# Optimization experiments

Hardware: AMD Instinct MI355X
Metric: run time of the kernel (lower is better)

The kernel has to match this reference:

```python
import jax, jax.numpy as jnp
import numpy as np

DX, DZ, DT = 10.0, 10.0, 1.0e-3
NX, NZ = 512, 512
NSTEPS, NREC = 512, 128
DT2 = DT * DT
INV_DXDZ = 1.0 / (DX * DZ)


def setup_inputs() -> dict:
    key = jax.random.key(0)
    k1, k2, k3, k4 = jax.random.split(key, 4)
    # velocity in [1500, 2500] m/s -> CFL stable with dt=1e-3, dx=dz=10
    velocity_model = 1500.0 + 1000.0 * jax.random.uniform(k1, (NX, NZ), dtype=jnp.float32)
    source = jax.random.normal(k2, (NSTEPS,), dtype=jnp.float32)
    rec_x = jax.random.randint(k3, (NREC,), 0, NX)
    rec_z = jax.random.randint(k4, (NREC,), 0, NZ)
    return {
        "velocity_model": velocity_model,
        "source": source,
        "src_x": 256,
        "src_z": 8,
        "rec_x": rec_x,
        "rec_z": rec_z,
    }


def _laplacian(p):
    # 3x3 cross stencil with zero padding, scaled by 1/(dx*dz) -- identical to
    # F.conv2d(p, [[0,1,0],[1,-4,1],[0,1,0]]/(dx*dz), padding=1)
    pp = jnp.pad(p, 1)
    return (pp[:-2, 1:-1] + pp[2:, 1:-1] + pp[1:-1, :-2] + pp[1:-1, 2:] - 4.0 * p) * INV_DXDZ


def reference(velocity_model, source, src_x, src_z, rec_x, rec_z):
    v2_dt2 = velocity_model * velocity_model * DT2  # [nx, nz]

    def step(carry, s_t):
        p, p_old = carry
        p_new = 2.0 * p - p_old + v2_dt2 * _laplacian(p)
        p_new = p_new.at[src_x, src_z].add(s_t * DT2)
        return (p_new, p), p_new[rec_x, rec_z]  # gather all receivers at once

    p0 = jnp.zeros((NX, NZ), dtype=velocity_model.dtype)
    _, recs = jax.lax.scan(step, (p0, p0), source)  # recs: [n_steps, n_rec]
    return recs.T  # seismogram: [n_rec, n_steps]
```

## Files before the change

kernel.cpp:

```cpp
#include <hip/hip_runtime.h>


#define NXd 512
#define NZd 512
#define NSTEPSd 512
#define NRECd 128
#define DT2f 1.0e-6f
#define INVf 1.0e-2f
#define TBk 16
#define TIk 32
#define EXTk 64
#define NTILEk 16
#define PADk 16
#define PWk 544
#define LROWS 66
#define NROUNDS (NSTEPSd / TBk)
#define MAXR 8

__device__ __forceinline__ float dpp_shr1(float x) {
    int v = __builtin_amdgcn_update_dpp(0, __builtin_bit_cast(int, x),
                                        0x138, 0xF, 0xF, false);
    return __builtin_bit_cast(float, v);
}
__device__ __forceinline__ float dpp_shl1(float x) {
    int v = __builtin_amdgcn_update_dpp(0, __builtin_bit_cast(int, x),
                                        0x130, 0xF, 0xF, false);
    return __builtin_bit_cast(float, v);
}

__device__ __forceinline__ float2 ldg_f2(const float2* p) {
    unsigned long long v = __hip_atomic_load(
        (const unsigned long long*)p, __ATOMIC_RELAXED, __HIP_MEMORY_SCOPE_AGENT);
    return __builtin_bit_cast(float2, v);
}
__device__ __forceinline__ float ldg_f1(const float* p) {
    unsigned v = __hip_atomic_load(
        (const unsigned*)p, __ATOMIC_RELAXED, __HIP_MEMORY_SCOPE_AGENT);
    return __builtin_bit_cast(float, v);
}
__device__ __forceinline__ void stg_f2(float2* p, float2 x) {
    __hip_atomic_store((unsigned long long*)p,
                       __builtin_bit_cast(unsigned long long, x),
                       __ATOMIC_RELAXED, __HIP_MEMORY_SCOPE_AGENT);
}

__global__ __launch_bounds__(1024) void fdtd_persist(
    const float* __restrict__ vel, const float* __restrict__ source,
    const int* __restrict__ src_x, const int* __restrict__ src_z,
    const int* __restrict__ rec_x, const int* __restrict__ rec_z,
    float2* __restrict__ PA, float2* __restrict__ PB,
    float* __restrict__ out, unsigned* __restrict__ done)
{
    __shared__ float sb[2][LROWS * EXTk];
    __shared__ int wflag[16 * 16];

    const int tid = threadIdx.x;
    const int w   = tid >> 6;
    const int ez  = tid & 63;
    const int bx = blockIdx.x, by = blockIdx.y;
    const int gx0 = by * TIk;
    const int gz0 = bx * TIk;
    const int ox = gx0 - TBk, oz = gz0 - TBk;
    const int myid = (by * NTILEk + bx) * 32;

    for (int i = tid; i < 34 * 34; i += 1024) {
        const int p = (by * 34 + i / 34) * PWk + (bx * 34 + i % 34);
        stg_f2(&PA[p], make_float2(0.f, 0.f));
        stg_f2(&PB[p], make_float2(0.f, 0.f));
    }

    int nR = 0; int rSlot[MAXR]; int rReg[MAXR];
    for (int r = 0; r < NRECd; ++r) {
        const int er = rec_x[r] - ox, ec = rec_z[r] - oz;
        if (er >= TBk && er < TBk + TIk && ec >= TBk && ec < TBk + TIk &&
            ec == ez && (er >> 2) == w && nR < MAXR) {
            rSlot[nR] = r; rReg[nR] = er & 3; ++nR;
        }
    }
    for (int j = 0; j < nR; ++j) {
        float4* o4 = (float4*)&out[rSlot[j] * NSTEPSd];
        for (int q = 0; q < NSTEPSd / 4; ++q) o4[q] = make_float4(0.f, 0.f, 0.f, 0.f);
    }

    float rV2i[4];
    {
        const int fz = oz + ez;
        #pragma unroll
        for (int i = 0; i < 4; ++i) {
            const int fx = ox + 4 * w + i;
            float v2 = 0.f;
            if (fx >= 0 && fx < NXd && fz >= 0 && fz < NZd) {
                float v = vel[fx * NZd + fz];
                v2 = v * v * (DT2f * INVf);
            }
            rV2i[i] = v2;
        }
    }

    if (w == 0) {
        sb[0][ez] = 0.f;
        sb[0][(LROWS - 1) * EXTk + ez] = 0.f;
        sb[1][ez] = 0.f;
        sb[1][(LROWS - 1) * EXTk + ez] = 0.f;
    }
    if (ez == 0) wflag[w * 16] = 0;

    const int sx = *src_x, sz = *src_z;
    const int exs = sx - ox, ezs = sz - oz;
    const bool srcHere = (exs >= 0 && exs < EXTk && ezs >= 0 && ezs < EXTk) &&
                         (tid == (((exs >> 2) << 6) | ezs));

    const int dxm = max(0, max(ox - sx, sx - (ox + EXTk - 1)));
    const int dzm = max(0, max(oz - sz, sz - (oz + EXTk - 1)));
    const int dman = dxm + dzm;
    const int kAct = dman <= (TBk + 1) ? 0 : (dman - (TBk + 1) + TBk - 1) / TBk;

    const int lane = tid & 63;
    int nb = myid;
    if (lane < 8) {
        const int d = (lane < 4) ? lane : lane + 1;
        const int ny = min(NTILEk - 1, max(0, by + d / 3 - 1));
        const int nx = min(NTILEk - 1, max(0, bx + d % 3 - 1));
        nb = (ny * NTILEk + nx) * 32;
    }

    const int pbase = (gx0 + 4 * w) * PWk + gz0 + ez;
    const int fbase = 4 * w * EXTk + ez;

    __syncthreads();
    if (tid == 0)
        __hip_atomic_store(&done[myid], (unsigned)(kAct + 1),
                           __ATOMIC_RELAXED, __HIP_MEMORY_SCOPE_AGENT);

    int base = 0;

    for (int k = kAct; k < NROUNDS; ++k) {
        const int t0 = TBk * k;

        if (lane < 8) {
            const unsigned tgt = (unsigned)(k + 1);
            for (;;) {
                unsigned seen = __hip_atomic_load(&done[nb], __ATOMIC_RELAXED,
                                                  __HIP_MEMORY_SCOPE_AGENT);
                if (seen >= tgt) break;
                if (seen + 1 < tgt) __builtin_amdgcn_s_sleep(16);
                else                __builtin_amdgcn_s_sleep(1);
            }
        }

        float2* __restrict__ Pin  = (k & 1) ? PB : PA;
        float2* __restrict__ Pout = (k & 1) ? PA : PB;

        float2 co[4];
        #pragma unroll
        for (int i = 0; i < 4; ++i) co[i] = ldg_f2(&Pin[pbase + i * PWk]);
        const float huG = ldg_f1((const float*)&Pin[pbase - PWk]);
        const float hdG = ldg_f1((const float*)&Pin[pbase + 4 * PWk]);

        float rCur[4], rOld[4];
        #pragma unroll
        for (int i = 0; i < 4; ++i) { rCur[i] = co[i].x; rOld[i] = co[i].y; }

        float sv[TBk];
        if (srcHere) {
            #pragma unroll
            for (int s = 0; s < TBk; ++s) sv[s] = source[t0 + s] * DT2f;
        }

        #pragma unroll
        for (int s = 0; s < TBk; ++s) {
            if (s > 0) {
                const int tgt = base + s;
                if (w > 0)
                    while (__hip_atomic_load(&wflag[(w - 1) * 16],
                                             __ATOMIC_ACQUIRE,
                                             __HIP_MEMORY_SCOPE_WORKGROUP) < tgt)
                        __builtin_amdgcn_s_sleep(1);
                if (w < 15)
                    while (__hip_atomic_load(&wflag[(w + 1) * 16],
                                             __ATOMIC_ACQUIRE,
                                             __HIP_MEMORY_SCOPE_WORKGROUP) < tgt)
                        __builtin_amdgcn_s_sleep(1);
            }
            const float* cur = sb[s & 1];
            float* nxt = sb[(s & 1) ^ 1];
            const float up0 = (s == 0) ? huG : cur[fbase];
            const float dn3 = (s == 0) ? hdG : cur[fbase + 5 * EXTk];
            float nv[4];
            #pragma unroll
            for (int i = 0; i < 4; ++i) {
                const float up = (i == 0) ? up0 : rCur[i - 1];
                const float dn = (i == 3) ? dn3 : rCur[i + 1];
                const float lf = dpp_shr1(rCur[i]);
                const float rt = dpp_shl1(rCur[i]);
                const float sum = (up + dn) + (lf + rt);
                const float t4 = __builtin_fmaf(-4.0f, rCur[i], sum);
                const float pm = __builtin_fmaf(2.0f, rCur[i], -rOld[i]);
                nv[i] = __builtin_fmaf(rV2i[i], t4, pm);
            }
            #pragma unroll
            for (int i = 0; i < 4; ++i) {
                rOld[i] = rCur[i];
                rCur[i] = nv[i];
                nxt[fbase + (1 + i) * EXTk] = nv[i];
            }
            if (srcHere) {
                #pragma unroll
                for (int i = 0; i < 4; ++i) {
                    if (i == (exs & 3)) {
                        rCur[i] += sv[s];
                        nxt[(exs + 1) * EXTk + ezs] = rCur[i];
                    }
                }
            }
            if (ez == 0)
                __hip_atomic_store(&wflag[w * 16], base + s + 1,
                                   __ATOMIC_RELEASE, __HIP_MEMORY_SCOPE_WORKGROUP);
            #pragma unroll
            for (int j = 0; j < MAXR; ++j) {
                if (j < nR) {
                    const int rr = rReg[j];
                    const float v = rr == 0 ? rCur[0] : rr == 1 ? rCur[1]
                                  : rr == 2 ? rCur[2] : rCur[3];
                    out[rSlot[j] * NSTEPSd + t0 + s] = v;
                }
            }
        }
        base += TBk;

        if (w >= 4 && w < 12 && ez >= TBk && ez < EXTk - TBk) {
            #pragma unroll
            for (int i = 0; i < 4; ++i)
                stg_f2(&Pout[pbase + i * PWk], make_float2(rCur[i], rOld[i]));
        }

        __syncthreads();
        if (tid == 0)
            __hip_atomic_store(&done[myid], (unsigned)(k + 2),
                               __ATOMIC_RELAXED, __HIP_MEMORY_SCOPE_AGENT);
    }
}

extern "C" void kernel_launch(void* const* d_in, const int* in_sizes, int n_in,
                              void* d_out, int out_size, void* d_ws, size_t ws_size,
                              hipStream_t stream) {
    const float* vel    = (const float*)d_in[0];
    const float* source = (const float*)d_in[1];
    const int*   src_x  = (const int*)d_in[2];
    const int*   src_z  = (const int*)d_in[3];
    const int*   rec_x  = (const int*)d_in[4];
    const int*   rec_z  = (const int*)d_in[5];
    float* out = (float*)d_out;

    const size_t FP = (size_t)PWk * PWk;
    float2* base = (float2*)d_ws;
    float2* PA = base + PWk;
    float2* PB = PA + FP;
    unsigned* DONE = (unsigned*)(PB + FP + PWk);

    hipMemsetAsync(DONE, 0, (size_t)NTILEk * NTILEk * 32 * sizeof(unsigned), stream);

    void* args[] = {(void*)&vel, (void*)&source, (void*)&src_x, (void*)&src_z,
                    (void*)&rec_x, (void*)&rec_z, (void*)&PA, (void*)&PB,
                    (void*)&out, (void*)&DONE};
    hipLaunchCooperativeKernel((void*)fdtd_persist, dim3(NTILEk, NTILEk),
                               dim3(1024), args, 0, stream);
}
```

Before: 392.1 us.

## Replace per-wave LDS flag spinning with block barrier and halo-only LDS exchange

Each wave now writes only its top and bottom rows (the halo rows neighbours need) into a compact LDS slot array, instead of all four rows. The point-to-point wave flags with acquire spin loops are replaced by a __syncthreads after every substep. The receiver-store loop is skipped when a thread owns no receivers. This cuts LDS traffic and flag polling, but the full-block barrier makes every wave wait for the slowest one each substep.

```diff
diff --git a/kernel.cpp b/kernel.cpp
--- a/kernel.cpp
+++ b/kernel.cpp
@@ -13,7 +13,7 @@
 #define NTILEk 16
 #define PADk 16
 #define PWk 544
-#define LROWS 66
+#define LSLOTS 34
 #define NROUNDS (NSTEPSd / TBk)
 #define MAXR 8
 
@@ -51,8 +51,7 @@
     float2* __restrict__ PA, float2* __restrict__ PB,
     float* __restrict__ out, unsigned* __restrict__ done)
 {
-    __shared__ float sb[2][LROWS * EXTk];
-    __shared__ int wflag[16 * 16];
+    __shared__ float sb[2][LSLOTS * EXTk];
 
     const int tid = threadIdx.x;
     const int w   = tid >> 6;
@@ -99,11 +98,10 @@
 
     if (w == 0) {
         sb[0][ez] = 0.f;
-        sb[0][(LROWS - 1) * EXTk + ez] = 0.f;
+        sb[0][(LSLOTS - 1) * EXTk + ez] = 0.f;
         sb[1][ez] = 0.f;
-        sb[1][(LROWS - 1) * EXTk + ez] = 0.f;
-    }
-    if (ez == 0) wflag[w * 16] = 0;
+        sb[1][(LSLOTS - 1) * EXTk + ez] = 0.f;
+    }
 
     const int sx = *src_x, sz = *src_z;
     const int exs = sx - ox, ezs = sz - oz;
@@ -125,14 +123,14 @@
     }
 
     const int pbase = (gx0 + 4 * w) * PWk + gz0 + ez;
-    const int fbase = 4 * w * EXTk + ez;
+    const int hbase = (2 * w) * EXTk + ez;
+    const int wb0   = (2 * w + 1) * EXTk + ez;
+    const int wb3   = (2 * w + 2) * EXTk + ez;
 
     __syncthreads();
     if (tid == 0)
         __hip_atomic_store(&done[myid], (unsigned)(kAct + 1),
                            __ATOMIC_RELAXED, __HIP_MEMORY_SCOPE_AGENT);
-
-    int base = 0;
 
     for (int k = kAct; k < NROUNDS; ++k) {
         const int t0 = TBk * k;
@@ -169,23 +167,10 @@
 
         #pragma unroll
         for (int s = 0; s < TBk; ++s) {
-            if (s > 0) {
-                const int tgt = base + s;
-                if (w > 0)
-                    while (__hip_atomic_load(&wflag[(w - 1) * 16],
-                                             __ATOMIC_ACQUIRE,
-                                             __HIP_MEMORY_SCOPE_WORKGROUP) < tgt)
-                        __builtin_amdgcn_s_sleep(1);
-                if (w < 15)
-                    while (__hip_atomic_load(&wflag[(w + 1) * 16],
-                                             __ATOMIC_ACQUIRE,
-                                             __HIP_MEMORY_SCOPE_WORKGROUP) < tgt)
-                        __builtin_amdgcn_s_sleep(1);
-            }
             const float* cur = sb[s & 1];
             float* nxt = sb[(s & 1) ^ 1];
-            const float up0 = (s == 0) ? huG : cur[fbase];
-            const float dn3 = (s == 0) ? hdG : cur[fbase + 5 * EXTk];
+            const float up0 = (s == 0) ? huG : cur[hbase];
+            const float dn3 = (s == 0) ? hdG : cur[hbase + 3 * EXTk];
             float nv[4];
             #pragma unroll
             for (int i = 0; i < 4; ++i) {
@@ -199,34 +184,32 @@
                 nv[i] = __builtin_fmaf(rV2i[i], t4, pm);
             }
             #pragma unroll
-            for (int i = 0; i < 4; ++i) {
-                rOld[i] = rCur[i];
-                rCur[i] = nv[i];
-                nxt[fbase + (1 + i) * EXTk] = nv[i];
-            }
+            for (int i = 0; i < 4; ++i) { rOld[i] = rCur[i]; rCur[i] = nv[i]; }
+            nxt[wb0] = nv[0];
+            nxt[wb3] = nv[3];
             if (srcHere) {
                 #pragma unroll
                 for (int i = 0; i < 4; ++i) {
                     if (i == (exs & 3)) {
                         rCur[i] += sv[s];
-                        nxt[(exs + 1) * EXTk + ezs] = rCur[i];
+                        if (i == 0) nxt[wb0] = rCur[0];
+                        if (i == 3) nxt[wb3] = rCur[3];
                     }
                 }
             }
-            if (ez == 0)
-                __hip_atomic_store(&wflag[w * 16], base + s + 1,
-                                   __ATOMIC_RELEASE, __HIP_MEMORY_SCOPE_WORKGROUP);
-            #pragma unroll
-            for (int j = 0; j < MAXR; ++j) {
-                if (j < nR) {
-                    const int rr = rReg[j];
-                    const float v = rr == 0 ? rCur[0] : rr == 1 ? rCur[1]
-                                  : rr == 2 ? rCur[2] : rCur[3];
-                    out[rSlot[j] * NSTEPSd + t0 + s] = v;
+            if (nR) {
+                #pragma unroll
+                for (int j = 0; j < MAXR; ++j) {
+                    if (j < nR) {
+                        const int rr = rReg[j];
+                        const float v = rr == 0 ? rCur[0] : rr == 1 ? rCur[1]
+                                      : rr == 2 ? rCur[2] : rCur[3];
+                        out[rSlot[j] * NSTEPSd + t0 + s] = v;
+                    }
                 }
             }
-        }
-        base += TBk;
+            __syncthreads();
+        }
 
         if (w >= 4 && w < 12 && ez >= TBk && ez < EXTk - TBk) {
             #pragma unroll
```

New measurement: 379.5 us. -3.2%, faster.
